# Kernel optimization log

Measured on AMD Instinct MI355X. Metric: run time of the kernel, lower is better.

Reference implementation:

```python
import jax, jax.numpy as jnp
import numpy as np
from jax import lax


def haar_dwt2(x):
    """Single-level 2D Haar (db1) DWT matching pywt sign conventions.
    x: (..., H, W) with H, W even. Returns (cA, cH, cV, cD) each (..., H/2, W/2).
    pywt db1: approx = (x0+x1)/sqrt2, detail = (x0-x1)/sqrt2; dwt2 keys:
    cH='da' (detail axis -2), cV='ad' (detail axis -1).
    """
    a = x[..., 0::2, 0::2]
    b = x[..., 0::2, 1::2]
    c = x[..., 1::2, 0::2]
    d = x[..., 1::2, 1::2]
    cA = (a + b + c + d) * 0.5
    cH = (a + b - c - d) * 0.5
    cV = (a - b + c - d) * 0.5
    cD = (a - b - c + d) * 0.5
    return cA, cH, cV, cD


def wavedec2_level2_array(x):
    """pywt.wavedec2(x, 'db1', level=2) followed by pywt.coeffs_to_array.
    x: (B, C, H, W) -> (B, C, H, W) coefficient array with layout:
      [[ [[cA2, cH2],[cV2, cD2]], cH1 ],
       [ cV1,                     cD1 ]]
    """
    cA1, cH1, cV1, cD1 = haar_dwt2(x)
    cA2, cH2, cV2, cD2 = haar_dwt2(cA1)
    lvl2 = jnp.concatenate([
        jnp.concatenate([cA2, cH2], axis=-1),
        jnp.concatenate([cV2, cD2], axis=-1),
    ], axis=-2)
    top = jnp.concatenate([lvl2, cH1], axis=-1)
    bot = jnp.concatenate([cV1, cD1], axis=-1)
    return jnp.concatenate([top, bot], axis=-2)


def setup_inputs() -> dict:
    key = jax.random.key(0)
    k1, k2, k3 = jax.random.split(key, 3)
    B, C, H = 128, 3, 224
    dim, patch = 768, 16
    x = jax.random.normal(k1, (B, C, H, H), dtype=jnp.float32)
    # Conv2d default init scale ~ 1/sqrt(fan_in)
    fan_in = C * patch * patch
    W = jax.random.normal(k2, (dim, C, patch, patch), dtype=jnp.float32) / np.sqrt(fan_in)
    b = jax.random.normal(k3, (dim,), dtype=jnp.float32) / np.sqrt(fan_in)
    return {"x": x, "W": W, "b": b}


def reference(x, W, b):
    patch = W.shape[-1]
    coeffs = wavedec2_level2_array(x)  # (B, C, H, W)
    y = lax.conv_general_dilated(
        coeffs, W,
        window_strides=(patch, patch),
        padding='VALID',
        dimension_numbers=('NCHW', 'OIHW', 'NCHW'),
    ) + b[None, :, None, None]          # (B, dim, H/p, W/p)
    B, D, Hp, Wp = y.shape
    return y.reshape(B, D, Hp * Wp).transpose(0, 2, 1)  # (B, seq, dim)
```

## Files before the change

### kernel.cpp

```cpp
#include <hip/hip_runtime.h>
#include <stdint.h>

typedef __attribute__((ext_vector_type(8))) __bf16 bf16x8;
typedef __attribute__((ext_vector_type(4))) float f32x4;

__device__ __forceinline__ unsigned short f2bf(float f) {
  union { float f; unsigned int u; } v; v.f = f;
  unsigned int u = v.u;
  return (unsigned short)((u + 0x7fffu + ((u >> 16) & 1u)) >> 16);
}

__device__ __forceinline__ void async_copy16(const void* g, void* s) {
  __builtin_amdgcn_global_load_lds(
      (__attribute__((address_space(1))) void*)const_cast<void*>(g),
      (__attribute__((address_space(3))) void*)s,
      16, 0, 0);
}

#define HAAR(a, bb, cc, dd, oA, oH, oV, oD)                                    \
  oA = 0.5f * ((a + bb) + (cc + dd));                                          \
  oH = 0.5f * ((a + bb) - (cc + dd));                                          \
  oV = 0.5f * ((a - bb) + (cc - dd));                                          \
  oD = 0.5f * ((a - bb) - (cc - dd));

__global__ __launch_bounds__(256) void convw_kernel(const float* __restrict__ W,
                                                    unsigned short* __restrict__ Wb) {
  int i = blockIdx.x * 256 + threadIdx.x;
  float4 v = ((const float4*)W)[i];
  uint2 o;
  o.x = (unsigned int)f2bf(v.x) | ((unsigned int)f2bf(v.y) << 16);
  o.y = (unsigned int)f2bf(v.z) | ((unsigned int)f2bf(v.w) << 16);
  ((uint2*)Wb)[i] = o;
}

__global__ __launch_bounds__(256) void dwt2_kernel(const float* __restrict__ x,
                                                   unsigned short* __restrict__ A) {
  int tid = blockIdx.x * 256 + threadIdx.x;
  int J = tid % 56;
  int t = tid / 56;
  int I = t % 56;
  t /= 56;
  int c = t % 3;
  int b = t / 3;

  const float* xp = x + (((size_t)t * 224 + 4 * I) * 224 + 4 * J);
  float4 r0 = *(const float4*)(xp);
  float4 r1 = *(const float4*)(xp + 224);
  float4 r2 = *(const float4*)(xp + 448);
  float4 r3 = *(const float4*)(xp + 672);

  float A1[2][2], H1[2][2], V1[2][2], D1[2][2];
  HAAR(r0.x, r0.y, r1.x, r1.y, A1[0][0], H1[0][0], V1[0][0], D1[0][0]);
  HAAR(r0.z, r0.w, r1.z, r1.w, A1[0][1], H1[0][1], V1[0][1], D1[0][1]);
  HAAR(r2.x, r2.y, r3.x, r3.y, A1[1][0], H1[1][0], V1[1][0], D1[1][0]);
  HAAR(r2.z, r2.w, r3.z, r3.w, A1[1][1], H1[1][1], V1[1][1], D1[1][1]);

  auto aidx = [&](int y, int xx) -> size_t {
    int mrow = b * 196 + (y >> 4) * 14 + (xx >> 4);
    int k = c * 256 + (y & 15) * 16 + (xx & 15);
    return (size_t)mrow * 768 + (size_t)k;
  };
  auto store2 = [&](int y, int xx, float v0, float v1) {
    unsigned int p = (unsigned int)f2bf(v0) | ((unsigned int)f2bf(v1) << 16);
    *(unsigned int*)(A + aidx(y, xx)) = p;
  };

  int y0 = 2 * I, x0 = 2 * J;
  store2(y0,           112 + x0, H1[0][0], H1[0][1]);
  store2(y0 + 1,       112 + x0, H1[1][0], H1[1][1]);
  store2(112 + y0,     x0,       V1[0][0], V1[0][1]);
  store2(112 + y0 + 1, x0,       V1[1][0], V1[1][1]);
  store2(112 + y0,     112 + x0, D1[0][0], D1[0][1]);
  store2(112 + y0 + 1, 112 + x0, D1[1][0], D1[1][1]);

  float vA2, vH2, vV2, vD2;
  HAAR(A1[0][0], A1[0][1], A1[1][0], A1[1][1], vA2, vH2, vV2, vD2);
  A[aidx(I,      J)]      = f2bf(vA2);
  A[aidx(I,      56 + J)] = f2bf(vH2);
  A[aidx(56 + I, J)]      = f2bf(vV2);
  A[aidx(56 + I, 56 + J)] = f2bf(vD2);
}

__global__ __launch_bounds__(256) void gemm_kernel(const unsigned short* __restrict__ A,
                                                   const unsigned short* __restrict__ Bt,
                                                   const float* __restrict__ bias,
                                                   float* __restrict__ C) {
  constexpr int K = 768, N = 768;
  constexpr int NT = 24;
  __shared__ unsigned short As[4][128 * 32];
  __shared__ unsigned short Bs[4][128 * 32];

  const int orig = blockIdx.x;
  const int tile = (orig & 7) * 147 + (orig >> 3);
  const int bm = tile / 6, bn = tile % 6;

  const int tid = threadIdx.x;
  const int lane = tid & 63;
  const int wave = tid >> 6;
  const int wr = wave >> 1, wc = wave & 1;
  const int mbase = bm * 128, nbase = bn * 128;

  f32x4 acc[4][4] = {};

  const int off0 = wave * 1024 + lane * 16;
  const int row0 = off0 >> 6;
  const int kc0 = (off0 >> 4) & 3;
  const int kcs = kc0 ^ ((row0 >> 1) & 3);
  const unsigned short* ga0 = A + (size_t)(mbase + row0) * K + kcs * 8;
  const unsigned short* ga1 = ga0 + (size_t)64 * K;
  const unsigned short* gb0 = Bt + (size_t)(nbase + row0) * K + kcs * 8;
  const unsigned short* gb1 = gb0 + (size_t)64 * K;

  auto stageA = [&](int buf, int kt) {
    char* sa = (char*)As + buf * 8192 + wave * 1024;
    async_copy16(ga0 + kt * 32, sa);
    async_copy16(ga1 + kt * 32, sa + 4096);
  };
  auto stageB = [&](int buf, int kt) {
    char* sb = (char*)Bs + buf * 8192 + wave * 1024;
    async_copy16(gb0 + kt * 32, sb);
    async_copy16(gb1 + kt * 32, sb + 4096);
  };

  const int fr = lane & 15;
  const int kq = lane >> 4;
  const int chq = kq ^ ((fr >> 1) & 3);

  stageA(0, 0); stageB(0, 0);
  stageA(1, 1); stageB(1, 1);
  stageA(2, 2); stageB(2, 2);
  asm volatile("s_waitcnt vmcnt(8)" ::: "memory");
  __builtin_amdgcn_s_barrier();

#pragma unroll
  for (int kt = 0; kt < NT; ++kt) {
    const int cb = kt & 3;
    const char* pa = (const char*)As + cb * 8192 + (wr * 64 + fr) * 64 + chq * 16;
    const char* pb = (const char*)Bs + cb * 8192 + (wc * 64 + fr) * 64 + chq * 16;
    bf16x8 af[4], bv[4];

    if (kt + 3 < NT) stageA((kt + 3) & 3, kt + 3);
#pragma unroll
    for (int ni = 0; ni < 4; ++ni) bv[ni] = *(const bf16x8*)(pb + ni * 1024);
    af[0] = *(const bf16x8*)(pa);
    af[1] = *(const bf16x8*)(pa + 1024);
    asm volatile("s_waitcnt lgkmcnt(0)" ::: "memory");
    __builtin_amdgcn_sched_barrier(0);
    __builtin_amdgcn_s_setprio(1);
#pragma unroll
    for (int mi = 0; mi < 2; ++mi)
#pragma unroll
      for (int ni = 0; ni < 4; ++ni)
        acc[mi][ni] = __builtin_amdgcn_mfma_f32_16x16x32_bf16(af[mi], bv[ni],
                                                              acc[mi][ni], 0, 0, 0);
    __builtin_amdgcn_s_setprio(0);

    if (kt + 3 < NT) stageB((kt + 3) & 3, kt + 3);
    af[2] = *(const bf16x8*)(pa + 2048);
    af[3] = *(const bf16x8*)(pa + 3072);
    asm volatile("s_waitcnt lgkmcnt(0)" ::: "memory");
    __builtin_amdgcn_sched_barrier(0);
    __builtin_amdgcn_s_setprio(1);
#pragma unroll
    for (int mi = 2; mi < 4; ++mi)
#pragma unroll
      for (int ni = 0; ni < 4; ++ni)
        acc[mi][ni] = __builtin_amdgcn_mfma_f32_16x16x32_bf16(af[mi], bv[ni],
                                                              acc[mi][ni], 0, 0, 0);
    __builtin_amdgcn_s_setprio(0);

    if (kt <= NT - 4)
      asm volatile("s_waitcnt vmcnt(8)" ::: "memory");
    else if (kt == NT - 3)
      asm volatile("s_waitcnt vmcnt(4)" ::: "memory");
    else if (kt == NT - 2)
      asm volatile("s_waitcnt vmcnt(0)" ::: "memory");
    if (kt < NT - 1) __builtin_amdgcn_s_barrier();
  }

  const int rq = lane >> 4;
#pragma unroll
  for (int ni = 0; ni < 4; ++ni) {
    int n = nbase + wc * 64 + ni * 16 + fr;
    float bv = bias[n];
#pragma unroll
    for (int mi = 0; mi < 4; ++mi) {
      int mrow = mbase + wr * 64 + mi * 16 + rq * 4;
      f32x4 v = acc[mi][ni];
#pragma unroll
      for (int j = 0; j < 4; ++j) C[(size_t)(mrow + j) * N + n] = v[j] + bv;
    }
  }
}

extern "C" void kernel_launch(void* const* d_in, const int* in_sizes, int n_in,
                              void* d_out, int out_size, void* d_ws, size_t ws_size,
                              hipStream_t stream) {
  const float* x = (const float*)d_in[0];
  const float* W = (const float*)d_in[1];
  const float* bias = (const float*)d_in[2];
  float* out = (float*)d_out;

  unsigned short* A = (unsigned short*)d_ws;
  unsigned short* Wb = (unsigned short*)((char*)d_ws + 38535168);

  convw_kernel<<<576, 256, 0, stream>>>(W, Wb);
  dwt2_kernel<<<4704, 256, 0, stream>>>(x, A);
  gemm_kernel<<<1176, 256, 0, stream>>>(A, Wb, bias, out);
}
```

Baseline: 73.04 us.

## Enlarge GEMM tile to 256x128 with 8 waves, BK=64, triple-buffered LDS

Restructures the GEMM so each 512-thread workgroup computes a 256x128 output tile with a 64-wide K step, using a 3-stage LDS ring instead of a 4-stage ring with K step 32. The goal is more operand reuse per LDS load, fewer loop iterations, and fewer workgroups, with an XCD-aware tile remap for the new 588-block grid. In exchange it uses more LDS (144KB per block) and adds a ping-pong barrier schedule that interleaves staging with MFMA phases, which may cost occupancy and add sync overhead.

New measurement: 81.16 us. 11.1% more time.

```diff
diff --git a/kernel.cpp b/kernel.cpp
--- a/kernel.cpp
+++ b/kernel.cpp
@@ -81,69 +81,69 @@
   A[aidx(56 + I, 56 + J)] = f2bf(vD2);
 }
 
-__global__ __launch_bounds__(256) void gemm_kernel(const unsigned short* __restrict__ A,
-                                                   const unsigned short* __restrict__ Bt,
-                                                   const float* __restrict__ bias,
-                                                   float* __restrict__ C) {
+__global__ __launch_bounds__(512, 2) void gemm_kernel(const unsigned short* __restrict__ A,
+                                                      const unsigned short* __restrict__ Bt,
+                                                      const float* __restrict__ bias,
+                                                      float* __restrict__ C) {
   constexpr int K = 768, N = 768;
-  constexpr int NT = 24;
-  __shared__ unsigned short As[4][128 * 32];
-  __shared__ unsigned short Bs[4][128 * 32];
+  constexpr int NT = 12;
+  __shared__ unsigned short As[3][256 * 64];
+  __shared__ unsigned short Bs[3][128 * 64];
 
   const int orig = blockIdx.x;
-  const int tile = (orig & 7) * 147 + (orig >> 3);
-  const int bm = tile / 6, bn = tile % 6;
+  const int xcd = orig & 7, idx = orig >> 3;
+  const int wgid = (xcd < 4 ? xcd * 74 : 296 + (xcd - 4) * 73) + idx;
+  const int bm = wgid / 6, bn = wgid % 6;
 
   const int tid = threadIdx.x;
   const int lane = tid & 63;
   const int wave = tid >> 6;
-  const int wr = wave >> 1, wc = wave & 1;
-  const int mbase = bm * 128, nbase = bn * 128;
+  const int wm = wave >> 1;
+  const int wn = wave & 1;
+  const int mbase = bm * 256, nbase = bn * 128;
 
   f32x4 acc[4][4] = {};
 
-  const int off0 = wave * 1024 + lane * 16;
-  const int row0 = off0 >> 6;
-  const int kc0 = (off0 >> 4) & 3;
-  const int kcs = kc0 ^ ((row0 >> 1) & 3);
-  const unsigned short* ga0 = A + (size_t)(mbase + row0) * K + kcs * 8;
-  const unsigned short* ga1 = ga0 + (size_t)64 * K;
-  const unsigned short* gb0 = Bt + (size_t)(nbase + row0) * K + kcs * 8;
-  const unsigned short* gb1 = gb0 + (size_t)64 * K;
-
-  auto stageA = [&](int buf, int kt) {
-    char* sa = (char*)As + buf * 8192 + wave * 1024;
-    async_copy16(ga0 + kt * 32, sa);
-    async_copy16(ga1 + kt * 32, sa + 4096);
-  };
-  auto stageB = [&](int buf, int kt) {
-    char* sb = (char*)Bs + buf * 8192 + wave * 1024;
-    async_copy16(gb0 + kt * 32, sb);
-    async_copy16(gb1 + kt * 32, sb + 4096);
+  const int lc = (lane & 7) ^ ((lane >> 3) & 7);
+  const int srow = wave * 8 + (lane >> 3);
+  const unsigned short* gA[4];
+  const unsigned short* gB[2];
+#pragma unroll
+  for (int i = 0; i < 4; ++i) gA[i] = A + (size_t)(mbase + i * 64 + srow) * K + lc * 8;
+#pragma unroll
+  for (int j = 0; j < 2; ++j) gB[j] = Bt + (size_t)(nbase + j * 64 + srow) * K + lc * 8;
+
+  auto stA = [&](int i, int buf, int kt) {
+    async_copy16(gA[i] + kt * 64, (char*)As + buf * 32768 + i * 8192 + wave * 1024);
+  };
+  auto stB = [&](int j, int buf, int kt) {
+    async_copy16(gB[j] + kt * 64, (char*)Bs + buf * 16384 + j * 8192 + wave * 1024);
   };
 
   const int fr = lane & 15;
   const int kq = lane >> 4;
-  const int chq = kq ^ ((fr >> 1) & 3);
-
-  stageA(0, 0); stageB(0, 0);
-  stageA(1, 1); stageB(1, 1);
-  stageA(2, 2); stageB(2, 2);
-  asm volatile("s_waitcnt vmcnt(8)" ::: "memory");
+  const int ch0 = ((kq) ^ (fr & 7)) * 16;
+  const int ch1 = ((4 + kq) ^ (fr & 7)) * 16;
+
+  stA(0, 0, 0); stA(1, 0, 0); stA(2, 0, 0); stA(3, 0, 0); stB(0, 0, 0); stB(1, 0, 0);
+  stA(0, 1, 1); stA(1, 1, 1); stA(2, 1, 1); stA(3, 1, 1); stB(0, 1, 1); stB(1, 1, 1);
+  asm volatile("s_waitcnt vmcnt(6)" ::: "memory");
   __builtin_amdgcn_s_barrier();
 
 #pragma unroll
   for (int kt = 0; kt < NT; ++kt) {
-    const int cb = kt & 3;
-    const char* pa = (const char*)As + cb * 8192 + (wr * 64 + fr) * 64 + chq * 16;
-    const char* pb = (const char*)Bs + cb * 8192 + (wc * 64 + fr) * 64 + chq * 16;
+    const int c = kt % 3, cs = (kt + 2) % 3;
+    const bool st = (kt + 2) < NT;
+    const char* paw = (const char*)As + c * 32768 + (wm * 64 + fr) * 128;
+    const char* pbw = (const char*)Bs + c * 16384 + (wn * 64 + fr) * 128;
     bf16x8 af[4], bv[4];
 
-    if (kt + 3 < NT) stageA((kt + 3) & 3, kt + 3);
-#pragma unroll
-    for (int ni = 0; ni < 4; ++ni) bv[ni] = *(const bf16x8*)(pb + ni * 1024);
-    af[0] = *(const bf16x8*)(pa);
-    af[1] = *(const bf16x8*)(pa + 1024);
+    if (st) { stA(0, cs, kt + 2); stA(1, cs, kt + 2); }
+#pragma unroll
+    for (int ni = 0; ni < 4; ++ni) bv[ni] = *(const bf16x8*)(pbw + ni * 2048 + ch0);
+    af[0] = *(const bf16x8*)(paw + ch0);
+    af[1] = *(const bf16x8*)(paw + 2048 + ch0);
+    __builtin_amdgcn_s_barrier();
     asm volatile("s_waitcnt lgkmcnt(0)" ::: "memory");
     __builtin_amdgcn_sched_barrier(0);
     __builtin_amdgcn_s_setprio(1);
@@ -154,10 +154,12 @@
         acc[mi][ni] = __builtin_amdgcn_mfma_f32_16x16x32_bf16(af[mi], bv[ni],
                                                               acc[mi][ni], 0, 0, 0);
     __builtin_amdgcn_s_setprio(0);
-
-    if (kt + 3 < NT) stageB((kt + 3) & 3, kt + 3);
-    af[2] = *(const bf16x8*)(pa + 2048);
-    af[3] = *(const bf16x8*)(pa + 3072);
+    __builtin_amdgcn_s_barrier();
+
+    if (st) { stA(2, cs, kt + 2); stA(3, cs, kt + 2); }
+    af[2] = *(const bf16x8*)(paw + 2 * 2048 + ch0);
+    af[3] = *(const bf16x8*)(paw + 3 * 2048 + ch0);
+    __builtin_amdgcn_s_barrier();
     asm volatile("s_waitcnt lgkmcnt(0)" ::: "memory");
     __builtin_amdgcn_sched_barrier(0);
     __builtin_amdgcn_s_setprio(1);
@@ -168,27 +170,60 @@
         acc[mi][ni] = __builtin_amdgcn_mfma_f32_16x16x32_bf16(af[mi], bv[ni],
                                                               acc[mi][ni], 0, 0, 0);
     __builtin_amdgcn_s_setprio(0);
-
-    if (kt <= NT - 4)
-      asm volatile("s_waitcnt vmcnt(8)" ::: "memory");
-    else if (kt == NT - 3)
-      asm volatile("s_waitcnt vmcnt(4)" ::: "memory");
-    else if (kt == NT - 2)
-      asm volatile("s_waitcnt vmcnt(0)" ::: "memory");
-    if (kt < NT - 1) __builtin_amdgcn_s_barrier();
+    __builtin_amdgcn_s_barrier();
+
+    if (st) stB(0, cs, kt + 2);
+#pragma unroll
+    for (int ni = 0; ni < 4; ++ni) bv[ni] = *(const bf16x8*)(pbw + ni * 2048 + ch1);
+    af[0] = *(const bf16x8*)(paw + ch1);
+    af[1] = *(const bf16x8*)(paw + 2048 + ch1);
+    __builtin_amdgcn_s_barrier();
+    asm volatile("s_waitcnt lgkmcnt(0)" ::: "memory");
+    __builtin_amdgcn_sched_barrier(0);
+    __builtin_amdgcn_s_setprio(1);
+#pragma unroll
+    for (int mi = 0; mi < 2; ++mi)
+#pragma unroll
+      for (int ni = 0; ni < 4; ++ni)
+        acc[mi][ni] = __builtin_amdgcn_mfma_f32_16x16x32_bf16(af[mi], bv[ni],
+                                                              acc[mi][ni], 0, 0, 0);
+    __builtin_amdgcn_s_setprio(0);
+    __builtin_amdgcn_s_barrier();
+
+    if (st) stB(1, cs, kt + 2);
+    af[2] = *(const bf16x8*)(paw + 2 * 2048 + ch1);
+    af[3] = *(const bf16x8*)(paw + 3 * 2048 + ch1);
+    __builtin_amdgcn_s_barrier();
+    asm volatile("s_waitcnt lgkmcnt(0)" ::: "memory");
+    __builtin_amdgcn_sched_barrier(0);
+    __builtin_amdgcn_s_setprio(1);
+#pragma unroll
+    for (int mi = 2; mi < 4; ++mi)
+#pragma unroll
+      for (int ni = 0; ni < 4; ++ni)
+        acc[mi][ni] = __builtin_amdgcn_mfma_f32_16x16x32_bf16(af[mi], bv[ni],
+                                                              acc[mi][ni], 0, 0, 0);
+    __builtin_amdgcn_s_setprio(0);
+    if (kt < NT - 1) {
+      if (st)
+        asm volatile("s_waitcnt vmcnt(6)" ::: "memory");
+      else
+        asm volatile("s_waitcnt vmcnt(0)" ::: "memory");
+      __builtin_amdgcn_s_barrier();
+    }
   }
 
   const int rq = lane >> 4;
 #pragma unroll
   for (int ni = 0; ni < 4; ++ni) {
-    int n = nbase + wc * 64 + ni * 16 + fr;
-    float bv = bias[n];
+    int n = nbase + wn * 64 + ni * 16 + fr;
+    float bb = bias[n];
 #pragma unroll
     for (int mi = 0; mi < 4; ++mi) {
-      int mrow = mbase + wr * 64 + mi * 16 + rq * 4;
+      int mrow = mbase + wm * 64 + mi * 16 + rq * 4;
       f32x4 v = acc[mi][ni];
 #pragma unroll
-      for (int j = 0; j < 4; ++j) C[(size_t)(mrow + j) * N + n] = v[j] + bv;
+      for (int j = 0; j < 4; ++j) C[(size_t)(mrow + j) * N + n] = v[j] + bb;
     }
   }
 }
@@ -206,5 +241,5 @@
 
   convw_kernel<<<576, 256, 0, stream>>>(W, Wb);
   dwt2_kernel<<<4704, 256, 0, stream>>>(x, A);
-  gemm_kernel<<<1176, 256, 0, stream>>>(A, Wb, bias, out);
-}
+  gemm_kernel<<<588, 512, 0, stream>>>(A, Wb, bias, out);
+}
```
